# Optimization experiments

Hardware: AMD Instinct MI355X
Metric: run time of the kernel (lower is better)

The kernel has to match this reference:

```python
import jax, jax.numpy as jnp
import numpy as np

N_NODES = 100000
N_EDGES = 1600000
D = 128


def setup_inputs() -> dict:
    key = jax.random.key(0)
    ks = jax.random.split(key, 9)
    inp = {
        "embs": jax.random.normal(ks[0], (N_NODES, D), dtype=jnp.float32),
        "edge_index0": jax.random.randint(ks[1], (2, N_EDGES), 0, N_NODES, dtype=jnp.int64 if jax.config.jax_enable_x64 else jnp.int32),
        "edge_index1": jax.random.randint(ks[2], (2, N_EDGES), 0, N_NODES, dtype=jnp.int64 if jax.config.jax_enable_x64 else jnp.int32),
        "w_l0": jax.random.normal(ks[3], (D, D), dtype=jnp.float32) * (1.0 / np.sqrt(D)),
        "w_r0": jax.random.normal(ks[4], (D, D), dtype=jnp.float32) * (1.0 / np.sqrt(D)),
        "b0": jnp.zeros((D,), dtype=jnp.float32),
        "w_l1": jax.random.normal(ks[5], (D, D), dtype=jnp.float32) * (1.0 / np.sqrt(D)),
        "w_r1": jax.random.normal(ks[6], (D, D), dtype=jnp.float32) * (1.0 / np.sqrt(D)),
        "b1": jnp.zeros((D,), dtype=jnp.float32),
    }
    return inp


def _sage_conv(x, edge_index, w_l, w_r, b):
    # PyG SAGEConv: out[i] = lin_l(mean_{j->i} x[j]) + lin_r(x[i])
    src, dst = edge_index[0], edge_index[1]
    n = x.shape[0]
    msg = jnp.take(x, src, axis=0)                                  # [E, D] gather
    summed = jax.ops.segment_sum(msg, dst, num_segments=n)          # [N, D] scatter-add
    cnt = jax.ops.segment_sum(jnp.ones(src.shape, x.dtype), dst, num_segments=n)
    agg = summed / jnp.maximum(cnt, 1.0)[:, None]                   # mean; 0 for isolated nodes
    return agg @ w_l.T + b + x @ w_r.T


def reference(embs, edge_index0, edge_index1, w_l0, w_r0, b0, w_l1, w_r1, b1):
    # layer 0 (not last): dropout (eval -> identity) + GELU (torch default = exact erf)
    x = _sage_conv(embs, edge_index0, w_l0, w_r0, b0)
    x = jax.nn.gelu(x, approximate=False)
    # layer 1 (last): no dropout / activation
    x = _sage_conv(x, edge_index1, w_l1, w_r1, b1)
    return x
```

## Files before the change

### kernel.cpp

```cpp
#include <hip/hip_runtime.h>
#include <hip/hip_fp16.h>
#include <math.h>

#define D 128
#define SH 9
#define BW (1 << SH)
#define EPT 16

typedef _Float16 half4v __attribute__((ext_vector_type(4)));
typedef _Float16 half8  __attribute__((ext_vector_type(8)));
typedef float    floatx16 __attribute__((ext_vector_type(16)));

typedef __attribute__((address_space(3))) uint32_t lds_u32_t;
typedef const __attribute__((address_space(1))) uint32_t g_u32_t;

__global__ __launch_bounds__(256) void cast_half(
        const float* __restrict__ x, _Float16* __restrict__ y, int n) {
    int i = blockIdx.x * 256 + threadIdx.x;
    int idx = i * 4;
    if (idx >= n) return;
    float4 v = *(const float4*)(x + idx);
    half4v h;
    h[0] = (_Float16)v.x; h[1] = (_Float16)v.y;
    h[2] = (_Float16)v.z; h[3] = (_Float16)v.w;
    *(half4v*)(y + idx) = h;
}

__global__ __launch_bounds__(256) void prep_bswz2(
        const float* __restrict__ wl0, const float* __restrict__ wr0,
        const float* __restrict__ wl1, const float* __restrict__ wr1,
        _Float16* __restrict__ B0, _Float16* __restrict__ B1) {
    int gid = blockIdx.x * 256 + threadIdx.x;
    if (gid >= 2 * 64 * 512) return;
    int layer = gid >> 15;
    int idx = gid & 32767;
    const float* wl = layer ? wl1 : wl0;
    const float* wr = layer ? wr1 : wr0;
    _Float16* B = layer ? B1 : B0;
    int j = idx & 7;
    int lane = (idx >> 3) & 63;
    int f = idx >> 9;
    int ks = f >> 2, cb = f & 3;
    int k = ks * 16 + (lane >> 5) * 8 + j;
    int c = cb * 32 + (lane & 31);
    float v = (k < 128) ? wl[c * 128 + k] : wr[c * 128 + (k - 128)];
    B[idx] = (_Float16)v;
}

__global__ __launch_bounds__(256) void hist_coarse(
        const int* __restrict__ ei0, const int* __restrict__ ei1,
        int E, int NBK, int* __restrict__ ccnt) {
    __shared__ int h[512];
    int NBIN = 2 * NBK;
    int t = threadIdx.x;
    h[t] = 0; h[t + 256] = 0;
    __syncthreads();
    int t0 = blockIdx.x * (256 * EPT) + t;
#pragma unroll
    for (int k = 0; k < EPT; ++k) {
        int idx = t0 + k * 256;
        if (idx < 2 * E) {
            int g = idx >= E;
            int e = idx - g * E;
            int dst = (g ? ei1 : ei0)[E + e];
            atomicAdd(&h[g * NBK + (dst >> SH)], 1);
        }
    }
    __syncthreads();
    for (int b = t; b < NBIN; b += 256)
        if (h[b]) atomicAdd(&ccnt[b * 16], h[b]);
}

__global__ __launch_bounds__(256) void scan_coarse(
        const int* __restrict__ ccnt, int NBK, int E, int N,
        int* __restrict__ gbase, int* __restrict__ gcur,
        int* __restrict__ rp0, int* __restrict__ rp1) {
    __shared__ int part[256];
    int t = threadIdx.x;
    for (int g = 0; g < 2; ++g) {
        int v = (t < NBK) ? ccnt[(g * NBK + t) * 16] : 0;
        part[t] = v;
        __syncthreads();
        for (int off = 1; off < 256; off <<= 1) {
            int u = (t >= off) ? part[t - off] : 0;
            __syncthreads();
            part[t] += u;
            __syncthreads();
        }
        if (t < NBK) {
            int ex = (t == 0) ? 0 : part[t - 1];
            int b = g * NBK + t;
            gbase[b] = ex;
            gcur[b * 16] = ex;
        }
        __syncthreads();
    }
    if (t == 0) { rp0[N] = E; rp1[N] = E; }
}

__global__ __launch_bounds__(256) void bin_pass1(
        const int* __restrict__ ei0, const int* __restrict__ ei1,
        int E, int NBK, int* __restrict__ gcur,
        int* __restrict__ stage0, int* __restrict__ stage1) {
    __shared__ int cnt[512];
    __shared__ int base[512];
    int NBIN = 2 * NBK;
    int t = threadIdx.x;
    cnt[t] = 0; cnt[t + 256] = 0;
    __syncthreads();
    int t0 = blockIdx.x * (256 * EPT) + t;
    int pk[EPT];
    int bn[EPT];
#pragma unroll
    for (int k = 0; k < EPT; ++k) {
        int idx = t0 + k * 256;
        bn[k] = -1;
        if (idx < 2 * E) {
            int g = idx >= E;
            int e = idx - g * E;
            const int* ei = g ? ei1 : ei0;
            int src = ei[e];
            int dst = ei[E + e];
            pk[k] = src | ((dst & (BW - 1)) << 17);
            bn[k] = g * NBK + (dst >> SH);
            atomicAdd(&cnt[bn[k]], 1);
        }
    }
    __syncthreads();
    for (int b = t; b < NBIN; b += 256) {
        int c = cnt[b];
        base[b] = c ? atomicAdd(&gcur[b * 16], c) : 0;
        cnt[b] = 0;
    }
    __syncthreads();
#pragma unroll
    for (int k = 0; k < EPT; ++k) {
        if (bn[k] >= 0) {
            int b = bn[k];
            int r = atomicAdd(&cnt[b], 1);
            int* stage = (b >= NBK) ? stage1 : stage0;
            stage[base[b] + r] = pk[k];
        }
    }
}

__global__ __launch_bounds__(256) void bin_pass2(
        const int* __restrict__ gbase,
        const int* __restrict__ stage0, const int* __restrict__ stage1,
        int* __restrict__ rp0, int* __restrict__ rp1,
        int* __restrict__ es0, int* __restrict__ es1,
        int N, int NBK, int E) {
    __shared__ int cnt[BW];
    __shared__ int part[256];
    int b = blockIdx.x;
    int g = b >= NBK;
    int bk = b - g * NBK;
    const int* stage = g ? stage1 : stage0;
    int* rp = g ? rp1 : rp0;
    int* es = g ? es1 : es0;
    int lo = bk << SH;
    int hi = min(lo + BW, N);
    int nd = hi - lo;
    int beg = gbase[b];
    int end = (bk == NBK - 1) ? E : gbase[b + 1];
    int t = threadIdx.x;
    cnt[t] = 0; cnt[t + 256] = 0;
    __syncthreads();
    for (int i = beg + t; i < end; i += 256)
        atomicAdd(&cnt[(unsigned)stage[i] >> 17], 1);
    __syncthreads();
    int c0 = cnt[t * 2], c1 = cnt[t * 2 + 1];
    part[t] = c0 + c1;
    __syncthreads();
    for (int off = 1; off < 256; off <<= 1) {
        int u = (t >= off) ? part[t - off] : 0;
        __syncthreads();
        part[t] += u;
        __syncthreads();
    }
    int ex = (t == 0) ? 0 : part[t - 1];
    int base0 = beg + ex;
    if (t * 2 < nd)     rp[lo + t * 2]     = base0;
    if (t * 2 + 1 < nd) rp[lo + t * 2 + 1] = base0 + c0;
    __syncthreads();
    cnt[t * 2] = base0;
    cnt[t * 2 + 1] = base0 + c0;
    __syncthreads();
    int i = beg + t;
    for (; i + 768 < end; i += 1024) {
        unsigned p0 = (unsigned)stage[i];
        unsigned p1 = (unsigned)stage[i + 256];
        unsigned p2 = (unsigned)stage[i + 512];
        unsigned p3 = (unsigned)stage[i + 768];
        int q0 = atomicAdd(&cnt[p0 >> 17], 1);
        int q1 = atomicAdd(&cnt[p1 >> 17], 1);
        int q2 = atomicAdd(&cnt[p2 >> 17], 1);
        int q3 = atomicAdd(&cnt[p3 >> 17], 1);
        es[q0] = p0 & 0x1FFFF;
        es[q1] = p1 & 0x1FFFF;
        es[q2] = p2 & 0x1FFFF;
        es[q3] = p3 & 0x1FFFF;
    }
    for (; i < end; i += 256) {
        unsigned p = (unsigned)stage[i];
        int q = atomicAdd(&cnt[p >> 17], 1);
        es[q] = p & 0x1FFFF;
    }
}

__device__ __forceinline__ float gelu_fast(float v) {
    float z = v * 0.70710678118654752f;
    float s = fabsf(z);
    float t = __builtin_amdgcn_rcpf(fmaf(0.3275911f, s, 1.0f));
    float poly = t * fmaf(t, fmaf(t, fmaf(t, fmaf(t, 1.061405429f,
                      -1.453152027f), 1.421413741f), -0.284496736f),
                      0.254829592f);
    float e = __builtin_amdgcn_exp2f(-1.4426950408889634f * s * s);
    float erfv = copysignf(fmaf(-poly, e, 1.0f), z);
    return 0.5f * v * (1.0f + erfv);
}

template <bool GELU, typename OutT>
__global__ __launch_bounds__(256, 3) void fused_sage(
        const _Float16* __restrict__ xsrc, const int* __restrict__ rp,
        const int* __restrict__ es, const _Float16* __restrict__ Bswz,
        const float* __restrict__ bias, OutT* __restrict__ out, int N) {
    __shared__ uint4 a_lds[32 * 65];

    const int tid = threadIdx.x;
    const int n0 = blockIdx.x * 64;
    const int wave = tid >> 6;
    const int lane = tid & 63;
    const int l31 = lane & 31;
    const int lhi = lane >> 5;

    if (n0 + 64 <= N) {
#pragma unroll
        for (int i = 0; i < 4; ++i) {
            int c = 16 + wave * 4 + i;
            int r0 = n0 + 4 * (c & 15);
            const char* g = (const char*)xsrc + (size_t)r0 * 256 + lane * 16;
            uint32_t* l = (uint32_t*)((char*)a_lds + c * 1040);
            __builtin_amdgcn_global_load_lds((g_u32_t*)g, (lds_u32_t*)l,
                                             16, 0, 0);
        }
    } else {
#pragma unroll
        for (int i = 0; i < 4; ++i) {
            int c = 16 + wave * 4 + i;
            int grow = n0 + 4 * (c & 15) + (lane >> 4);
            uint4 v = make_uint4(0u, 0u, 0u, 0u);
            if (grow < N)
                v = *(const uint4*)((const char*)xsrc + (size_t)grow * 256
                                    + (lane & 15) * 16);
            *(uint4*)((char*)a_lds + c * 1040 + lane * 16) = v;
        }
    }

    half8 breg[2][8];
#pragma unroll
    for (int ph = 0; ph < 2; ++ph)
#pragma unroll
        for (int ks = 0; ks < 8; ++ks)
            breg[ph][ks] = *(const half8*)(
                Bswz + (size_t)ph * 16384 + ((ks * 4) + wave) * 512 + lane * 8);
#pragma unroll
    for (int ph = 0; ph < 2; ++ph)
#pragma unroll
        for (int ks = 0; ks < 8; ++ks)
            asm volatile("" : "+v"(breg[ph][ks]));

    {
        int nb = n0 + wave * 16;
        int rpi = min(nb + lane, N);
        int rpv = (lane < 17) ? rp[rpi] : 0;
        const char* xb = (const char*)xsrc;
        int grp = lane >> 5;
        unsigned co = (unsigned)l31 * 8u;
        float one = 1.0f;
        for (int k = 0; k < 16; ++k) {
            int beg = __shfl(rpv, k);
            int end = __shfl(rpv, k + 1);
            float ax = 0.f, ay = 0.f, az = 0.f, aw = 0.f;
            for (int chunk = beg; chunk < end; chunk += 64) {
                int n = min(64, end - chunk);
                int iv = (lane < n) ? es[chunk + lane] : -1;
                for (int e = 0; e < n; e += 8) {
                    int s[4];
                    uint2 v[4];
#pragma unroll
                    for (int j = 0; j < 4; ++j)
                        s[j] = __shfl(iv, e + 2 * j + grp);
#pragma unroll
                    for (int j = 0; j < 4; ++j) {
                        v[j] = make_uint2(0u, 0u);
                        if (s[j] >= 0)
                            v[j] = *(const uint2*)(xb + (unsigned)s[j] * 256u
                                                   + co);
                    }
#pragma unroll
                    for (int j = 0; j < 4; ++j) {
                        asm("v_fma_mix_f32 %0, %1, %2, %0 op_sel:[0,0,0] op_sel_hi:[1,0,0]"
                            : "+v"(ax) : "v"(v[j].x), "v"(one));
                        asm("v_fma_mix_f32 %0, %1, %2, %0 op_sel:[1,0,0] op_sel_hi:[1,0,0]"
                            : "+v"(ay) : "v"(v[j].x), "v"(one));
                        asm("v_fma_mix_f32 %0, %1, %2, %0 op_sel:[0,0,0] op_sel_hi:[1,0,0]"
                            : "+v"(az) : "v"(v[j].y), "v"(one));
                        asm("v_fma_mix_f32 %0, %1, %2, %0 op_sel:[1,0,0] op_sel_hi:[1,0,0]"
                            : "+v"(aw) : "v"(v[j].y), "v"(one));
                    }
                }
            }
            ax += __shfl_xor(ax, 32);
            ay += __shfl_xor(ay, 32);
            az += __shfl_xor(az, 32);
            aw += __shfl_xor(aw, 32);
            int deg = end - beg;
            float inv = (deg > 0) ? 1.0f / (float)deg : 0.0f;
            if (lane < 32) {
                half4v h;
                h[0] = (_Float16)(ax * inv);
                h[1] = (_Float16)(ay * inv);
                h[2] = (_Float16)(az * inv);
                h[3] = (_Float16)(aw * inv);
                int r = wave * 16 + k;
                *(half4v*)((char*)a_lds + (r >> 2) * 1040 + (r & 3) * 256
                           + co) = h;
            }
        }
    }

    floatx16 acc[2];
#pragma unroll
    for (int r2 = 0; r2 < 2; ++r2)
#pragma unroll
        for (int r = 0; r < 16; ++r) acc[r2][r] = 0.0f;

    __syncthreads();

#pragma unroll
    for (int ph = 0; ph < 2; ++ph)
#pragma unroll
        for (int ks = 0; ks < 8; ++ks)
#pragma unroll
            for (int r2 = 0; r2 < 2; ++r2) {
                int r = ph * 64 + r2 * 32 + l31;
                int abyte = (r >> 2) * 1040 + (r & 3) * 256
                            + ks * 32 + lhi * 16;
                half8 af = *(const half8*)((const char*)a_lds + abyte);
                acc[r2] = __builtin_amdgcn_mfma_f32_32x32x16_f16(
                    af, breg[ph][ks], acc[r2], 0, 0, 0);
            }

    {
        int col = wave * 32 + l31;
        float bv = bias[col];
#pragma unroll
        for (int r2 = 0; r2 < 2; ++r2)
#pragma unroll
            for (int r = 0; r < 16; ++r) {
                int rowin = (r & 3) + 8 * (r >> 2) + 4 * lhi;
                int grow = n0 + r2 * 32 + rowin;
                if (grow < N) {
                    float v = acc[r2][r] + bv;
                    if (GELU) v = gelu_fast(v);
                    out[(size_t)grow * 128 + col] = (OutT)v;
                }
            }
    }
}

extern "C" void kernel_launch(void* const* d_in, const int* in_sizes, int n_in,
                              void* d_out, int out_size, void* d_ws, size_t ws_size,
                              hipStream_t stream) {
    const float* embs = (const float*)d_in[0];
    const int*   ei0  = (const int*)d_in[1];
    const int*   ei1  = (const int*)d_in[2];
    const float* w_l0 = (const float*)d_in[3];
    const float* w_r0 = (const float*)d_in[4];
    const float* b0   = (const float*)d_in[5];
    const float* w_l1 = (const float*)d_in[6];
    const float* w_r1 = (const float*)d_in[7];
    const float* b1   = (const float*)d_in[8];
    float* out = (float*)d_out;

    const int N = in_sizes[0] / D;
    const int E = in_sizes[1] / 2;
    const int NBK = (N + BW - 1) >> SH;
    const int NBIN = 2 * NBK;

    _Float16* x_h   = (_Float16*)d_ws;
    _Float16* h_h   = x_h + (size_t)N * D;
    _Float16* agg_h = h_h + (size_t)N * D;
    _Float16* Bswz0 = agg_h + (size_t)N * D;
    _Float16* Bswz1 = Bswz0 + 64 * 512;
    int* rp0   = (int*)(Bswz1 + 64 * 512);
    int* rp1   = rp0 + (N + 1);
    int* es0   = rp1 + (N + 1);
    int* es1   = es0 + E;
    int* ccnt  = es1 + E;
    int* gbase = ccnt + NBIN * 16;
    int* gcur  = gbase + NBIN;
    int* stage0 = (int*)agg_h;
    int* stage1 = stage0 + E;

    const int cast_grid = ((size_t)N * D / 4 + 255) / 256;
    const int bin_grid  = (2 * E + 256 * EPT - 1) / (256 * EPT);
    const int gemm_grid = (N + 63) / 64;

    cast_half<<<cast_grid, 256, 0, stream>>>(embs, x_h, N * D);
    prep_bswz2<<<256, 256, 0, stream>>>(w_l0, w_r0, w_l1, w_r1, Bswz0, Bswz1);

    hipMemsetAsync(ccnt, 0, (size_t)NBIN * 16 * sizeof(int), stream);
    hist_coarse<<<bin_grid, 256, 0, stream>>>(ei0, ei1, E, NBK, ccnt);
    scan_coarse<<<1, 256, 0, stream>>>(ccnt, NBK, E, N, gbase, gcur, rp0, rp1);
    bin_pass1<<<bin_grid, 256, 0, stream>>>(ei0, ei1, E, NBK, gcur,
                                            stage0, stage1);
    bin_pass2<<<NBIN, 256, 0, stream>>>(gbase, stage0, stage1,
                                        rp0, rp1, es0, es1, N, NBK, E);

    fused_sage<true, _Float16><<<gemm_grid, 256, 0, stream>>>(
        x_h, rp0, es0, Bswz0, b0, h_h, N);

    fused_sage<false, float><<<gemm_grid, 256, 0, stream>>>(
        h_h, rp1, es1, Bswz1, b1, out, N);
}
```

Before: 391.1 us.

## Widen gather loads to 16 bytes, defer second weight load, raise occupancy

New measurement: 385.0 us. Within noise of the previous version (-1.6%).

```diff
diff --git a/kernel.cpp b/kernel.cpp
--- a/kernel.cpp
+++ b/kernel.cpp
@@ -220,8 +220,15 @@
     return 0.5f * v * (1.0f + erfv);
 }
 
+#define FMA_MIX_LO(acc, src) \
+    asm("v_fma_mix_f32 %0, %1, %2, %0 op_sel:[0,0,0] op_sel_hi:[1,0,0]" \
+        : "+v"(acc) : "v"(src), "v"(one))
+#define FMA_MIX_HI(acc, src) \
+    asm("v_fma_mix_f32 %0, %1, %2, %0 op_sel:[1,0,0] op_sel_hi:[1,0,0]" \
+        : "+v"(acc) : "v"(src), "v"(one))
+
 template <bool GELU, typename OutT>
-__global__ __launch_bounds__(256, 3) void fused_sage(
+__global__ __launch_bounds__(256, 4) void fused_sage(
         const _Float16* __restrict__ xsrc, const int* __restrict__ rp,
         const int* __restrict__ es, const _Float16* __restrict__ Bswz,
         const float* __restrict__ bias, OutT* __restrict__ out, int N) {
@@ -257,75 +264,76 @@
         }
     }
 
-    half8 breg[2][8];
-#pragma unroll
-    for (int ph = 0; ph < 2; ++ph)
-#pragma unroll
-        for (int ks = 0; ks < 8; ++ks)
-            breg[ph][ks] = *(const half8*)(
-                Bswz + (size_t)ph * 16384 + ((ks * 4) + wave) * 512 + lane * 8);
-#pragma unroll
-    for (int ph = 0; ph < 2; ++ph)
-#pragma unroll
-        for (int ks = 0; ks < 8; ++ks)
-            asm volatile("" : "+v"(breg[ph][ks]));
+    half8 breg0[8];
+#pragma unroll
+    for (int ks = 0; ks < 8; ++ks)
+        breg0[ks] = *(const half8*)(
+            Bswz + ((ks * 4) + wave) * 512 + lane * 8);
+#pragma unroll
+    for (int ks = 0; ks < 8; ++ks)
+        asm volatile("" : "+v"(breg0[ks]));
 
     {
         int nb = n0 + wave * 16;
         int rpi = min(nb + lane, N);
         int rpv = (lane < 17) ? rp[rpi] : 0;
         const char* xb = (const char*)xsrc;
-        int grp = lane >> 5;
-        unsigned co = (unsigned)l31 * 8u;
+        int g4 = lane >> 4;
+        int li = lane & 15;
+        unsigned co = (unsigned)li * 16u;
         float one = 1.0f;
         for (int k = 0; k < 16; ++k) {
             int beg = __shfl(rpv, k);
             int end = __shfl(rpv, k + 1);
-            float ax = 0.f, ay = 0.f, az = 0.f, aw = 0.f;
+            float a0 = 0.f, a1 = 0.f, a2 = 0.f, a3 = 0.f;
+            float a4 = 0.f, a5 = 0.f, a6 = 0.f, a7 = 0.f;
             for (int chunk = beg; chunk < end; chunk += 64) {
                 int n = min(64, end - chunk);
                 int iv = (lane < n) ? es[chunk + lane] : -1;
-                for (int e = 0; e < n; e += 8) {
+                for (int e = 0; e < n; e += 16) {
                     int s[4];
-                    uint2 v[4];
-#pragma unroll
-                    for (int j = 0; j < 4; ++j)
-                        s[j] = __shfl(iv, e + 2 * j + grp);
+                    uint4 v[4];
 #pragma unroll
                     for (int j = 0; j < 4; ++j) {
-                        v[j] = make_uint2(0u, 0u);
+                        int ei_ = e + j * 4 + g4;
+                        int sv = __shfl(iv, ei_);
+                        s[j] = (ei_ < n) ? sv : -1;
+                    }
+#pragma unroll
+                    for (int j = 0; j < 4; ++j) {
+                        v[j] = make_uint4(0u, 0u, 0u, 0u);
                         if (s[j] >= 0)
-                            v[j] = *(const uint2*)(xb + (unsigned)s[j] * 256u
+                            v[j] = *(const uint4*)(xb + (unsigned)s[j] * 256u
                                                    + co);
                     }
 #pragma unroll
                     for (int j = 0; j < 4; ++j) {
-                        asm("v_fma_mix_f32 %0, %1, %2, %0 op_sel:[0,0,0] op_sel_hi:[1,0,0]"
-                            : "+v"(ax) : "v"(v[j].x), "v"(one));
-                        asm("v_fma_mix_f32 %0, %1, %2, %0 op_sel:[1,0,0] op_sel_hi:[1,0,0]"
-                            : "+v"(ay) : "v"(v[j].x), "v"(one));
-                        asm("v_fma_mix_f32 %0, %1, %2, %0 op_sel:[0,0,0] op_sel_hi:[1,0,0]"
-                            : "+v"(az) : "v"(v[j].y), "v"(one));
-                        asm("v_fma_mix_f32 %0, %1, %2, %0 op_sel:[1,0,0] op_sel_hi:[1,0,0]"
-                            : "+v"(aw) : "v"(v[j].y), "v"(one));
+                        FMA_MIX_LO(a0, v[j].x); FMA_MIX_HI(a1, v[j].x);
+                        FMA_MIX_LO(a2, v[j].y); FMA_MIX_HI(a3, v[j].y);
+                        FMA_MIX_LO(a4, v[j].z); FMA_MIX_HI(a5, v[j].z);
+                        FMA_MIX_LO(a6, v[j].w); FMA_MIX_HI(a7, v[j].w);
                     }
                 }
             }
-            ax += __shfl_xor(ax, 32);
-            ay += __shfl_xor(ay, 32);
-            az += __shfl_xor(az, 32);
-            aw += __shfl_xor(aw, 32);
+            a0 += __shfl_xor(a0, 16); a1 += __shfl_xor(a1, 16);
+            a2 += __shfl_xor(a2, 16); a3 += __shfl_xor(a3, 16);
+            a4 += __shfl_xor(a4, 16); a5 += __shfl_xor(a5, 16);
+            a6 += __shfl_xor(a6, 16); a7 += __shfl_xor(a7, 16);
+            a0 += __shfl_xor(a0, 32); a1 += __shfl_xor(a1, 32);
+            a2 += __shfl_xor(a2, 32); a3 += __shfl_xor(a3, 32);
+            a4 += __shfl_xor(a4, 32); a5 += __shfl_xor(a5, 32);
+            a6 += __shfl_xor(a6, 32); a7 += __shfl_xor(a7, 32);
             int deg = end - beg;
             float inv = (deg > 0) ? 1.0f / (float)deg : 0.0f;
-            if (lane < 32) {
-                half4v h;
-                h[0] = (_Float16)(ax * inv);
-                h[1] = (_Float16)(ay * inv);
-                h[2] = (_Float16)(az * inv);
-                h[3] = (_Float16)(aw * inv);
+            if (g4 == 0) {
+                half8 h;
+                h[0] = (_Float16)(a0 * inv); h[1] = (_Float16)(a1 * inv);
+                h[2] = (_Float16)(a2 * inv); h[3] = (_Float16)(a3 * inv);
+                h[4] = (_Float16)(a4 * inv); h[5] = (_Float16)(a5 * inv);
+                h[6] = (_Float16)(a6 * inv); h[7] = (_Float16)(a7 * inv);
                 int r = wave * 16 + k;
-                *(half4v*)((char*)a_lds + (r >> 2) * 1040 + (r & 3) * 256
-                           + co) = h;
+                *(half8*)((char*)a_lds + (r >> 2) * 1040 + (r & 3) * 256
+                          + co) = h;
             }
         }
     }
@@ -338,19 +346,35 @@
 
     __syncthreads();
 
-#pragma unroll
-    for (int ph = 0; ph < 2; ++ph)
-#pragma unroll
-        for (int ks = 0; ks < 8; ++ks)
-#pragma unroll
-            for (int r2 = 0; r2 < 2; ++r2) {
-                int r = ph * 64 + r2 * 32 + l31;
-                int abyte = (r >> 2) * 1040 + (r & 3) * 256
-                            + ks * 32 + lhi * 16;
-                half8 af = *(const half8*)((const char*)a_lds + abyte);
-                acc[r2] = __builtin_amdgcn_mfma_f32_32x32x16_f16(
-                    af, breg[ph][ks], acc[r2], 0, 0, 0);
-            }
+    half8 breg1[8];
+#pragma unroll
+    for (int ks = 0; ks < 8; ++ks)
+        breg1[ks] = *(const half8*)(
+            Bswz + 16384 + ((ks * 4) + wave) * 512 + lane * 8);
+#pragma unroll
+    for (int ks = 0; ks < 8; ++ks)
+        asm volatile("" : "+v"(breg1[ks]));
+
+#pragma unroll
+    for (int ks = 0; ks < 8; ++ks)
+#pragma unroll
+        for (int r2 = 0; r2 < 2; ++r2) {
+            int r = r2 * 32 + l31;
+            int abyte = (r >> 2) * 1040 + (r & 3) * 256 + ks * 32 + lhi * 16;
+            half8 af = *(const half8*)((const char*)a_lds + abyte);
+            acc[r2] = __builtin_amdgcn_mfma_f32_32x32x16_f16(
+                af, breg0[ks], acc[r2], 0, 0, 0);
+        }
+#pragma unroll
+    for (int ks = 0; ks < 8; ++ks)
+#pragma unroll
+        for (int r2 = 0; r2 < 2; ++r2) {
+            int r = 64 + r2 * 32 + l31;
+            int abyte = (r >> 2) * 1040 + (r & 3) * 256 + ks * 32 + lhi * 16;
+            half8 af = *(const half8*)((const char*)a_lds + abyte);
+            acc[r2] = __builtin_amdgcn_mfma_f32_32x32x16_f16(
+                af, breg1[ks], acc[r2], 0, 0, 0);
+        }
 
     {
         int col = wave * 32 + l31;
```

## Halve LDS and drop register-resident B to double occupancy in fused SAGE

Applied to the files above, without the earlier changes.

Measured after the change: 413.3 us. 1.06x slower.

```diff
diff --git a/kernel.cpp b/kernel.cpp
--- a/kernel.cpp
+++ b/kernel.cpp
@@ -220,12 +220,19 @@
     return 0.5f * v * (1.0f + erfv);
 }
 
+#define FMA_MIX_LO(acc, src) \
+    asm("v_fma_mix_f32 %0, %1, %2, %0 op_sel:[0,0,0] op_sel_hi:[1,0,0]" \
+        : "+v"(acc) : "v"(src), "v"(one))
+#define FMA_MIX_HI(acc, src) \
+    asm("v_fma_mix_f32 %0, %1, %2, %0 op_sel:[1,0,0] op_sel_hi:[1,0,0]" \
+        : "+v"(acc) : "v"(src), "v"(one))
+
 template <bool GELU, typename OutT>
-__global__ __launch_bounds__(256, 3) void fused_sage(
+__global__ __launch_bounds__(256, 6) void fused_sage(
         const _Float16* __restrict__ xsrc, const int* __restrict__ rp,
         const int* __restrict__ es, const _Float16* __restrict__ Bswz,
         const float* __restrict__ bias, OutT* __restrict__ out, int N) {
-    __shared__ uint4 a_lds[32 * 65];
+    __shared__ uint4 a_lds[16 * 65];
 
     const int tid = threadIdx.x;
     const int n0 = blockIdx.x * 64;
@@ -233,42 +240,6 @@
     const int lane = tid & 63;
     const int l31 = lane & 31;
     const int lhi = lane >> 5;
-
-    if (n0 + 64 <= N) {
-#pragma unroll
-        for (int i = 0; i < 4; ++i) {
-            int c = 16 + wave * 4 + i;
-            int r0 = n0 + 4 * (c & 15);
-            const char* g = (const char*)xsrc + (size_t)r0 * 256 + lane * 16;
-            uint32_t* l = (uint32_t*)((char*)a_lds + c * 1040);
-            __builtin_amdgcn_global_load_lds((g_u32_t*)g, (lds_u32_t*)l,
-                                             16, 0, 0);
-        }
-    } else {
-#pragma unroll
-        for (int i = 0; i < 4; ++i) {
-            int c = 16 + wave * 4 + i;
-            int grow = n0 + 4 * (c & 15) + (lane >> 4);
-            uint4 v = make_uint4(0u, 0u, 0u, 0u);
-            if (grow < N)
-                v = *(const uint4*)((const char*)xsrc + (size_t)grow * 256
-                                    + (lane & 15) * 16);
-            *(uint4*)((char*)a_lds + c * 1040 + lane * 16) = v;
-        }
-    }
-
-    half8 breg[2][8];
-#pragma unroll
-    for (int ph = 0; ph < 2; ++ph)
-#pragma unroll
-        for (int ks = 0; ks < 8; ++ks)
-            breg[ph][ks] = *(const half8*)(
-                Bswz + (size_t)ph * 16384 + ((ks * 4) + wave) * 512 + lane * 8);
-#pragma unroll
-    for (int ph = 0; ph < 2; ++ph)
-#pragma unroll
-        for (int ks = 0; ks < 8; ++ks)
-            asm volatile("" : "+v"(breg[ph][ks]));
 
     {
         int nb = n0 + wave * 16;
@@ -300,14 +271,8 @@
                     }
 #pragma unroll
                     for (int j = 0; j < 4; ++j) {
-                        asm("v_fma_mix_f32 %0, %1, %2, %0 op_sel:[0,0,0] op_sel_hi:[1,0,0]"
-                            : "+v"(ax) : "v"(v[j].x), "v"(one));
-                        asm("v_fma_mix_f32 %0, %1, %2, %0 op_sel:[1,0,0] op_sel_hi:[1,0,0]"
-                            : "+v"(ay) : "v"(v[j].x), "v"(one));
-                        asm("v_fma_mix_f32 %0, %1, %2, %0 op_sel:[0,0,0] op_sel_hi:[1,0,0]"
-                            : "+v"(az) : "v"(v[j].y), "v"(one));
-                        asm("v_fma_mix_f32 %0, %1, %2, %0 op_sel:[1,0,0] op_sel_hi:[1,0,0]"
-                            : "+v"(aw) : "v"(v[j].y), "v"(one));
+                        FMA_MIX_LO(ax, v[j].x); FMA_MIX_HI(ay, v[j].x);
+                        FMA_MIX_LO(az, v[j].y); FMA_MIX_HI(aw, v[j].y);
                     }
                 }
             }
@@ -339,18 +304,36 @@
     __syncthreads();
 
 #pragma unroll
-    for (int ph = 0; ph < 2; ++ph)
-#pragma unroll
-        for (int ks = 0; ks < 8; ++ks)
-#pragma unroll
-            for (int r2 = 0; r2 < 2; ++r2) {
-                int r = ph * 64 + r2 * 32 + l31;
-                int abyte = (r >> 2) * 1040 + (r & 3) * 256
-                            + ks * 32 + lhi * 16;
-                half8 af = *(const half8*)((const char*)a_lds + abyte);
-                acc[r2] = __builtin_amdgcn_mfma_f32_32x32x16_f16(
-                    af, breg[ph][ks], acc[r2], 0, 0, 0);
-            }
+    for (int ks = 0; ks < 8; ++ks) {
+        half8 bf = *(const half8*)(Bswz + ((ks * 4) + wave) * 512 + lane * 8);
+#pragma unroll
+        for (int r2 = 0; r2 < 2; ++r2) {
+            int r = r2 * 32 + l31;
+            int abyte = (r >> 2) * 1040 + (r & 3) * 256 + ks * 32 + lhi * 16;
+            half8 af = *(const half8*)((const char*)a_lds + abyte);
+            acc[r2] = __builtin_amdgcn_mfma_f32_32x32x16_f16(
+                af, bf, acc[r2], 0, 0, 0);
+        }
+    }
+
+#pragma unroll
+    for (int ks = 0; ks < 8; ++ks) {
+        half8 bf = *(const half8*)(Bswz + 16384 + ((ks * 4) + wave) * 512
+                                   + lane * 8);
+#pragma unroll
+        for (int r2 = 0; r2 < 2; ++r2) {
+            int grow = n0 + r2 * 32 + l31;
+            half8 af;
+            if (grow < N)
+                af = *(const half8*)(xsrc + (size_t)grow * 128
+                                     + ks * 16 + lhi * 8);
+            else
+#pragma unroll
+                for (int j = 0; j < 8; ++j) af[j] = (_Float16)0.f;
+            acc[r2] = __builtin_amdgcn_mfma_f32_32x32x16_f16(
+                af, bf, acc[r2], 0, 0, 0);
+        }
+    }
 
     {
         int col = wave * 32 + l31;
```

## Merge CSR build into one cooperative kernel and fuse prologue casts

Applied to the files above, without the earlier changes.

After: 720.3 us. +84.2%, slower.

```diff
diff --git a/kernel.cpp b/kernel.cpp
--- a/kernel.cpp
+++ b/kernel.cpp
@@ -1,6 +1,9 @@
 #include <hip/hip_runtime.h>
 #include <hip/hip_fp16.h>
+#include <hip/hip_cooperative_groups.h>
 #include <math.h>
+
+namespace cg = cooperative_groups;
 
 #define D 128
 #define SH 9
@@ -14,101 +17,62 @@
 typedef __attribute__((address_space(3))) uint32_t lds_u32_t;
 typedef const __attribute__((address_space(1))) uint32_t g_u32_t;
 
-__global__ __launch_bounds__(256) void cast_half(
-        const float* __restrict__ x, _Float16* __restrict__ y, int n) {
-    int i = blockIdx.x * 256 + threadIdx.x;
-    int idx = i * 4;
-    if (idx >= n) return;
-    float4 v = *(const float4*)(x + idx);
-    half4v h;
-    h[0] = (_Float16)v.x; h[1] = (_Float16)v.y;
-    h[2] = (_Float16)v.z; h[3] = (_Float16)v.w;
-    *(half4v*)(y + idx) = h;
-}
-
-__global__ __launch_bounds__(256) void prep_bswz2(
+__global__ __launch_bounds__(256) void prologue(
+        const float* __restrict__ x, _Float16* __restrict__ y, int n,
         const float* __restrict__ wl0, const float* __restrict__ wr0,
         const float* __restrict__ wl1, const float* __restrict__ wr1,
-        _Float16* __restrict__ B0, _Float16* __restrict__ B1) {
-    int gid = blockIdx.x * 256 + threadIdx.x;
-    if (gid >= 2 * 64 * 512) return;
-    int layer = gid >> 15;
-    int idx = gid & 32767;
-    const float* wl = layer ? wl1 : wl0;
-    const float* wr = layer ? wr1 : wr0;
-    _Float16* B = layer ? B1 : B0;
-    int j = idx & 7;
-    int lane = (idx >> 3) & 63;
-    int f = idx >> 9;
-    int ks = f >> 2, cb = f & 3;
-    int k = ks * 16 + (lane >> 5) * 8 + j;
-    int c = cb * 32 + (lane & 31);
-    float v = (k < 128) ? wl[c * 128 + k] : wr[c * 128 + (k - 128)];
-    B[idx] = (_Float16)v;
+        _Float16* __restrict__ B0, _Float16* __restrict__ B1, int cast_grid) {
+    if ((int)blockIdx.x < cast_grid) {
+        int i = blockIdx.x * 256 + threadIdx.x;
+        int idx = i * 4;
+        if (idx >= n) return;
+        float4 v = *(const float4*)(x + idx);
+        half4v h;
+        h[0] = (_Float16)v.x; h[1] = (_Float16)v.y;
+        h[2] = (_Float16)v.z; h[3] = (_Float16)v.w;
+        *(half4v*)(y + idx) = h;
+    } else {
+        int gid = (blockIdx.x - cast_grid) * 256 + threadIdx.x;
+        if (gid >= 2 * 64 * 512) return;
+        int layer = gid >> 15;
+        int idx = gid & 32767;
+        const float* wl = layer ? wl1 : wl0;
+        const float* wr = layer ? wr1 : wr0;
+        _Float16* B = layer ? B1 : B0;
+        int j = idx & 7;
+        int lane = (idx >> 3) & 63;
+        int f = idx >> 9;
+        int ks = f >> 2, cb = f & 3;
+        int k = ks * 16 + (lane >> 5) * 8 + j;
+        int c = cb * 32 + (lane & 31);
+        float v = (k < 128) ? wl[c * 128 + k] : wr[c * 128 + (k - 128)];
+        B[idx] = (_Float16)v;
+    }
 }
 
-__global__ __launch_bounds__(256) void hist_coarse(
+__global__ __launch_bounds__(256) void csr_coop(
         const int* __restrict__ ei0, const int* __restrict__ ei1,
-        int E, int NBK, int* __restrict__ ccnt) {
-    __shared__ int h[512];
-    int NBIN = 2 * NBK;
-    int t = threadIdx.x;
-    h[t] = 0; h[t + 256] = 0;
-    __syncthreads();
-    int t0 = blockIdx.x * (256 * EPT) + t;
-#pragma unroll
-    for (int k = 0; k < EPT; ++k) {
-        int idx = t0 + k * 256;
-        if (idx < 2 * E) {
-            int g = idx >= E;
-            int e = idx - g * E;
-            int dst = (g ? ei1 : ei0)[E + e];
-            atomicAdd(&h[g * NBK + (dst >> SH)], 1);
-        }
-    }
-    __syncthreads();
-    for (int b = t; b < NBIN; b += 256)
-        if (h[b]) atomicAdd(&ccnt[b * 16], h[b]);
-}
-
-__global__ __launch_bounds__(256) void scan_coarse(
-        const int* __restrict__ ccnt, int NBK, int E, int N,
-        int* __restrict__ gbase, int* __restrict__ gcur,
-        int* __restrict__ rp0, int* __restrict__ rp1) {
-    __shared__ int part[256];
-    int t = threadIdx.x;
-    for (int g = 0; g < 2; ++g) {
-        int v = (t < NBK) ? ccnt[(g * NBK + t) * 16] : 0;
-        part[t] = v;
-        __syncthreads();
-        for (int off = 1; off < 256; off <<= 1) {
-            int u = (t >= off) ? part[t - off] : 0;
-            __syncthreads();
-            part[t] += u;
-            __syncthreads();
-        }
-        if (t < NBK) {
-            int ex = (t == 0) ? 0 : part[t - 1];
-            int b = g * NBK + t;
-            gbase[b] = ex;
-            gcur[b * 16] = ex;
-        }
-        __syncthreads();
-    }
-    if (t == 0) { rp0[N] = E; rp1[N] = E; }
-}
-
-__global__ __launch_bounds__(256) void bin_pass1(
-        const int* __restrict__ ei0, const int* __restrict__ ei1,
-        int E, int NBK, int* __restrict__ gcur,
+        int E, int N, int NBK,
+        int* __restrict__ ccnt, int* __restrict__ gbase,
+        int* __restrict__ gcur,
+        int* __restrict__ rp0, int* __restrict__ rp1,
+        int* __restrict__ es0, int* __restrict__ es1,
         int* __restrict__ stage0, int* __restrict__ stage1) {
+    cg::grid_group grid = cg::this_grid();
     __shared__ int cnt[512];
     __shared__ int base[512];
-    int NBIN = 2 * NBK;
-    int t = threadIdx.x;
+    __shared__ int part[256];
+    const int NBIN = 2 * NBK;
+    const int t = threadIdx.x;
+    const int b = blockIdx.x;
+    const int nb = gridDim.x;
+
+    for (int i = b * 256 + t; i < NBIN * 16; i += nb * 256) ccnt[i] = 0;
+    grid.sync();
+
     cnt[t] = 0; cnt[t + 256] = 0;
     __syncthreads();
-    int t0 = blockIdx.x * (256 * EPT) + t;
+    int t0 = b * (256 * EPT) + t;
     int pk[EPT];
     int bn[EPT];
 #pragma unroll
@@ -127,84 +91,104 @@
         }
     }
     __syncthreads();
-    for (int b = t; b < NBIN; b += 256) {
-        int c = cnt[b];
-        base[b] = c ? atomicAdd(&gcur[b * 16], c) : 0;
-        cnt[b] = 0;
+    for (int bb = t; bb < NBIN; bb += 256)
+        if (cnt[bb]) atomicAdd(&ccnt[bb * 16], cnt[bb]);
+    grid.sync();
+
+    if (b == 0) {
+        for (int g = 0; g < 2; ++g) {
+            int v = (t < NBK) ? ccnt[(g * NBK + t) * 16] : 0;
+            part[t] = v;
+            __syncthreads();
+            for (int off = 1; off < 256; off <<= 1) {
+                int u = (t >= off) ? part[t - off] : 0;
+                __syncthreads();
+                part[t] += u;
+                __syncthreads();
+            }
+            if (t < NBK) {
+                int ex = (t == 0) ? 0 : part[t - 1];
+                int bk = g * NBK + t;
+                gbase[bk] = ex;
+                gcur[bk * 16] = ex;
+            }
+            __syncthreads();
+        }
+        if (t == 0) { rp0[N] = E; rp1[N] = E; }
+    }
+    grid.sync();
+
+    for (int bb = t; bb < NBIN; bb += 256) {
+        int c = cnt[bb];
+        base[bb] = c ? atomicAdd(&gcur[bb * 16], c) : 0;
+        cnt[bb] = 0;
     }
     __syncthreads();
 #pragma unroll
     for (int k = 0; k < EPT; ++k) {
         if (bn[k] >= 0) {
-            int b = bn[k];
-            int r = atomicAdd(&cnt[b], 1);
-            int* stage = (b >= NBK) ? stage1 : stage0;
-            stage[base[b] + r] = pk[k];
-        }
-    }
-}
-
-__global__ __launch_bounds__(256) void bin_pass2(
-        const int* __restrict__ gbase,
-        const int* __restrict__ stage0, const int* __restrict__ stage1,
-        int* __restrict__ rp0, int* __restrict__ rp1,
-        int* __restrict__ es0, int* __restrict__ es1,
-        int N, int NBK, int E) {
-    __shared__ int cnt[BW];
-    __shared__ int part[256];
-    int b = blockIdx.x;
-    int g = b >= NBK;
-    int bk = b - g * NBK;
-    const int* stage = g ? stage1 : stage0;
-    int* rp = g ? rp1 : rp0;
-    int* es = g ? es1 : es0;
-    int lo = bk << SH;
-    int hi = min(lo + BW, N);
-    int nd = hi - lo;
-    int beg = gbase[b];
-    int end = (bk == NBK - 1) ? E : gbase[b + 1];
-    int t = threadIdx.x;
-    cnt[t] = 0; cnt[t + 256] = 0;
-    __syncthreads();
-    for (int i = beg + t; i < end; i += 256)
-        atomicAdd(&cnt[(unsigned)stage[i] >> 17], 1);
-    __syncthreads();
-    int c0 = cnt[t * 2], c1 = cnt[t * 2 + 1];
-    part[t] = c0 + c1;
-    __syncthreads();
-    for (int off = 1; off < 256; off <<= 1) {
-        int u = (t >= off) ? part[t - off] : 0;
+            int bk = bn[k];
+            int r = atomicAdd(&cnt[bk], 1);
+            int* stage = (bk >= NBK) ? stage1 : stage0;
+            stage[base[bk] + r] = pk[k];
+        }
+    }
+    grid.sync();
+
+    if (b >= NBIN) return;
+    {
+        int g = b >= NBK;
+        int bk = b - g * NBK;
+        const int* stage = g ? stage1 : stage0;
+        int* rp = g ? rp1 : rp0;
+        int* es = g ? es1 : es0;
+        int lo = bk << SH;
+        int hi = min(lo + BW, N);
+        int nd = hi - lo;
+        int beg = gbase[b];
+        int end = (bk == NBK - 1) ? E : gbase[b + 1];
+        cnt[t] = 0; cnt[t + 256] = 0;
         __syncthreads();
-        part[t] += u;
+        for (int i = beg + t; i < end; i += 256)
+            atomicAdd(&cnt[(unsigned)stage[i] >> 17], 1);
         __syncthreads();
-    }
-    int ex = (t == 0) ? 0 : part[t - 1];
-    int base0 = beg + ex;
-    if (t * 2 < nd)     rp[lo + t * 2]     = base0;
-    if (t * 2 + 1 < nd) rp[lo + t * 2 + 1] = base0 + c0;
-    __syncthreads();
-    cnt[t * 2] = base0;
-    cnt[t * 2 + 1] = base0 + c0;
-    __syncthreads();
-    int i = beg + t;
-    for (; i + 768 < end; i += 1024) {
-        unsigned p0 = (unsigned)stage[i];
-        unsigned p1 = (unsigned)stage[i + 256];
-        unsigned p2 = (unsigned)stage[i + 512];
-        unsigned p3 = (unsigned)stage[i + 768];
-        int q0 = atomicAdd(&cnt[p0 >> 17], 1);
-        int q1 = atomicAdd(&cnt[p1 >> 17], 1);
-        int q2 = atomicAdd(&cnt[p2 >> 17], 1);
-        int q3 = atomicAdd(&cnt[p3 >> 17], 1);
-        es[q0] = p0 & 0x1FFFF;
-        es[q1] = p1 & 0x1FFFF;
-        es[q2] = p2 & 0x1FFFF;
-        es[q3] = p3 & 0x1FFFF;
-    }
-    for (; i < end; i += 256) {
-        unsigned p = (unsigned)stage[i];
-        int q = atomicAdd(&cnt[p >> 17], 1);
-        es[q] = p & 0x1FFFF;
+        int c0 = cnt[t * 2], c1 = cnt[t * 2 + 1];
+        part[t] = c0 + c1;
+        __syncthreads();
+        for (int off = 1; off < 256; off <<= 1) {
+            int u = (t >= off) ? part[t - off] : 0;
+            __syncthreads();
+            part[t] += u;
+            __syncthreads();
+        }
+        int ex = (t == 0) ? 0 : part[t - 1];
+        int base0 = beg + ex;
+        if (t * 2 < nd)     rp[lo + t * 2]     = base0;
+        if (t * 2 + 1 < nd) rp[lo + t * 2 + 1] = base0 + c0;
+        __syncthreads();
+        cnt[t * 2] = base0;
+        cnt[t * 2 + 1] = base0 + c0;
+        __syncthreads();
+        int i = beg + t;
+        for (; i + 768 < end; i += 1024) {
+            unsigned p0 = (unsigned)stage[i];
+            unsigned p1 = (unsigned)stage[i + 256];
+            unsigned p2 = (unsigned)stage[i + 512];
+            unsigned p3 = (unsigned)stage[i + 768];
+            int q0 = atomicAdd(&cnt[p0 >> 17], 1);
+            int q1 = atomicAdd(&cnt[p1 >> 17], 1);
+            int q2 = atomicAdd(&cnt[p2 >> 17], 1);
+            int q3 = atomicAdd(&cnt[p3 >> 17], 1);
+            es[q0] = p0 & 0x1FFFF;
+            es[q1] = p1 & 0x1FFFF;
+            es[q2] = p2 & 0x1FFFF;
+            es[q3] = p3 & 0x1FFFF;
+        }
+        for (; i < end; i += 256) {
+            unsigned p = (unsigned)stage[i];
+            int q = atomicAdd(&cnt[p >> 17], 1);
+            es[q] = p & 0x1FFFF;
+        }
     }
 }
 
@@ -219,6 +203,13 @@
     float erfv = copysignf(fmaf(-poly, e, 1.0f), z);
     return 0.5f * v * (1.0f + erfv);
 }
+
+#define FMA_MIX_LO(acc, src) \
+    asm("v_fma_mix_f32 %0, %1, %2, %0 op_sel:[0,0,0] op_sel_hi:[1,0,0]" \
+        : "+v"(acc) : "v"(src), "v"(one))
+#define FMA_MIX_HI(acc, src) \
+    asm("v_fma_mix_f32 %0, %1, %2, %0 op_sel:[1,0,0] op_sel_hi:[1,0,0]" \
+        : "+v"(acc) : "v"(src), "v"(one))
 
 template <bool GELU, typename OutT>
 __global__ __launch_bounds__(256, 3) void fused_sage(
@@ -300,14 +291,8 @@
                     }
 #pragma unroll
                     for (int j = 0; j < 4; ++j) {
-                        asm("v_fma_mix_f32 %0, %1, %2, %0 op_sel:[0,0,0] op_sel_hi:[1,0,0]"
-                            : "+v"(ax) : "v"(v[j].x), "v"(one));
-                        asm("v_fma_mix_f32 %0, %1, %2, %0 op_sel:[1,0,0] op_sel_hi:[1,0,0]"
-                            : "+v"(ay) : "v"(v[j].x), "v"(one));
-                        asm("v_fma_mix_f32 %0, %1, %2, %0 op_sel:[0,0,0] op_sel_hi:[1,0,0]"
-                            : "+v"(az) : "v"(v[j].y), "v"(one));
-                        asm("v_fma_mix_f32 %0, %1, %2, %0 op_sel:[1,0,0] op_sel_hi:[1,0,0]"
-                            : "+v"(aw) : "v"(v[j].y), "v"(one));
+                        FMA_MIX_LO(ax, v[j].x); FMA_MIX_HI(ay, v[j].x);
+                        FMA_MIX_LO(az, v[j].y); FMA_MIX_HI(aw, v[j].y);
                     }
                 }
             }
@@ -408,16 +393,22 @@
     const int bin_grid  = (2 * E + 256 * EPT - 1) / (256 * EPT);
     const int gemm_grid = (N + 63) / 64;
 
-    cast_half<<<cast_grid, 256, 0, stream>>>(embs, x_h, N * D);
-    prep_bswz2<<<256, 256, 0, stream>>>(w_l0, w_r0, w_l1, w_r1, Bswz0, Bswz1);
-
-    hipMemsetAsync(ccnt, 0, (size_t)NBIN * 16 * sizeof(int), stream);
-    hist_coarse<<<bin_grid, 256, 0, stream>>>(ei0, ei1, E, NBK, ccnt);
-    scan_coarse<<<1, 256, 0, stream>>>(ccnt, NBK, E, N, gbase, gcur, rp0, rp1);
-    bin_pass1<<<bin_grid, 256, 0, stream>>>(ei0, ei1, E, NBK, gcur,
-                                            stage0, stage1);
-    bin_pass2<<<NBIN, 256, 0, stream>>>(gbase, stage0, stage1,
-                                        rp0, rp1, es0, es1, N, NBK, E);
+    int n_elems = N * D;
+    prologue<<<cast_grid + 256, 256, 0, stream>>>(
+        embs, x_h, n_elems, w_l0, w_r0, w_l1, w_r1, Bswz0, Bswz1, cast_grid);
+
+    {
+        int E_ = E, N_ = N, NBK_ = NBK;
+        void* args[] = {
+            (void*)&ei0, (void*)&ei1, (void*)&E_, (void*)&N_, (void*)&NBK_,
+            (void*)&ccnt, (void*)&gbase, (void*)&gcur,
+            (void*)&rp0, (void*)&rp1, (void*)&es0, (void*)&es1,
+            (void*)&stage0, (void*)&stage1,
+        };
+        hipLaunchCooperativeKernel((const void*)csr_coop,
+                                   dim3(bin_grid), dim3(256),
+                                   args, 0, stream);
+    }
 
     fused_sage<true, _Float16><<<gemm_grid, 256, 0, stream>>>(
         x_h, rp0, es0, Bswz0, b0, h_h, N);
```
